# Kernel tuning notes

Measured on AMD Instinct MI355X. Metric: run time of the kernel, lower is better.

Reference implementation:

```python
import jax, jax.numpy as jnp
import numpy as np

N = 50000      # nodes
DEG = 16       # incoming edges per node
E = N * DEG    # edges
F = 256        # nfeat
H = 8          # heads
DH = 32        # nhid // nheads
ALPHA = 0.2    # LeakyReLU negative slope


def setup_inputs() -> dict:
    key = jax.random.key(0)
    ks = jax.random.split(key, 6)
    h = jax.random.normal(ks[0], (N, F), jnp.float32)
    # xavier_uniform-like scale for W (gain 1.414)
    lim_w = 1.414 * np.sqrt(6.0 / (F + DH))
    W = jax.random.uniform(ks[1], (H, F, DH), jnp.float32, -lim_w, lim_w)
    bW = jnp.zeros((H, DH), jnp.float32)
    lim_a = 1.414 * np.sqrt(6.0 / (2 * DH + 1))
    a_src = jax.random.uniform(ks[2], (H, DH), jnp.float32, -lim_a, lim_a)
    a_dst = jax.random.uniform(ks[3], (H, DH), jnp.float32, -lim_a, lim_a)
    a_bias = jnp.zeros((H,), jnp.float32)
    src = jax.random.randint(ks[4], (E,), 0, N, dtype=jnp.int32)
    # every node gets exactly DEG incoming edges (ensures non-empty mailbox)
    dst = jnp.repeat(jnp.arange(N, dtype=jnp.int32), DEG)
    return {"h": h, "W": W, "bW": bW, "a_src": a_src, "a_dst": a_dst,
            "a_bias": a_bias, "src": src, "dst": dst}


def reference(h, W, bW, a_src, a_dst, a_bias, src, dst):
    # per-head projection: Wh[n,h,d]
    Wh = jnp.einsum('nf,hfd->nhd', h, W) + bW
    # decomposed attention linear: a([Wh_src, Wh_dst]) = s1[src] + s2[dst] + b
    s1 = jnp.einsum('nhd,hd->nh', Wh, a_src)   # [N,H]
    s2 = jnp.einsum('nhd,hd->nh', Wh, a_dst)   # [N,H]
    e = jax.nn.leaky_relu(s1[src] + s2[dst] + a_bias, ALPHA)  # [E,H]
    # segment softmax over incoming edges per destination node
    m = jax.ops.segment_max(e, dst, num_segments=N)           # [N,H]
    ex = jnp.exp(e - m[dst])
    denom = jax.ops.segment_sum(ex, dst, num_segments=N)      # [N,H]
    attn = ex / denom[dst]                                    # [E,H]
    # weighted scatter-sum aggregation of source features
    hp = jax.ops.segment_sum(attn[:, :, None] * Wh[src], dst, num_segments=N)  # [N,H,DH]
    # concat heads (matches torch.cat over head outputs)
    return hp.reshape(N, H * DH)
```

## Files before the change

kernel.cpp:

```cpp
#include <hip/hip_runtime.h>

#define NNODES 50000
#define FEAT 256
#define NH 8
#define DHEAD 32
#define DEG 16
#define CDIM 256

typedef __attribute__((ext_vector_type(4))) float floatx4;
typedef __attribute__((ext_vector_type(8))) short shortx8;
typedef __attribute__((ext_vector_type(8))) unsigned short ushortx8;
typedef __attribute__((ext_vector_type(4))) int intx4;
typedef __attribute__((ext_vector_type(4))) _Float16 halfx4;

__device__ __forceinline__ unsigned short f2bf(float f) {
  union { float f; unsigned u; } v; v.f = f;
  unsigned r = v.u + 0x7fffu + ((v.u >> 16) & 1u);
  return (unsigned short)(r >> 16);
}
__device__ __forceinline__ float bf2f(unsigned short b) {
  union { unsigned u; float f; } v; v.u = ((unsigned)b) << 16;
  return v.f;
}

__global__ __launch_bounds__(256) void convert_wt(
    const float* __restrict__ W, unsigned short* __restrict__ Wt2) {
  int t = blockIdx.x * 256 + threadIdx.x;
#pragma unroll
  for (int p = 0; p < 4; ++p) {
    int idx = t * 4 + p;
    int jj = idx & 7;
    int l = (idx >> 3) & 63;
    int kt = (idx >> 9) & 7;
    int cgrp = idx >> 12;
    int c = cgrp * 16 + (l & 15);
    int f = kt * 32 + ((l >> 4) << 3) + jj;
    Wt2[idx] = f2bf(W[(size_t)(c >> 5) * (FEAT * DHEAD) + (size_t)f * DHEAD + (c & 31)]);
  }
}

__global__ __launch_bounds__(256) void gemm_fused(
    const float* __restrict__ h, const unsigned short* __restrict__ Wt2,
    const float* __restrict__ bW, const float* __restrict__ a_src,
    const float* __restrict__ a_dst, const float* __restrict__ a_bias,
    unsigned short* __restrict__ Whb, float* __restrict__ s1g,
    float* __restrict__ s2g) {
  __shared__ unsigned short As2[8 * 2 * 64 * 8];
  const int tid = threadIdx.x;
  const int w = tid >> 6, lane = tid & 63;
  const int mrow = lane & 15, quad = lane >> 4;
  const int row0 = blockIdx.x * 32;

  {
    int r2 = w & 1;
    int ktb = (w >> 1) * 4;
    int grow = row0 + r2 * 16 + mrow;
    if (grow > NNODES - 1) grow = NNODES - 1;
    const float* hp = h + (size_t)grow * FEAT + quad * 8;
#pragma unroll
    for (int ktl = 0; ktl < 4; ++ktl) {
      int kt = ktb + ktl;
      floatx4 v0 = __builtin_nontemporal_load((const floatx4*)(hp + kt * 32));
      floatx4 v1 = __builtin_nontemporal_load((const floatx4*)(hp + kt * 32 + 4));
      shortx8 a8;
      a8[0] = (short)f2bf(v0[0]); a8[1] = (short)f2bf(v0[1]);
      a8[2] = (short)f2bf(v0[2]); a8[3] = (short)f2bf(v0[3]);
      a8[4] = (short)f2bf(v1[0]); a8[5] = (short)f2bf(v1[1]);
      a8[6] = (short)f2bf(v1[2]); a8[7] = (short)f2bf(v1[3]);
      *(shortx8*)&As2[((kt * 2 + r2) * 64 + lane) * 8] = a8;
    }
  }
  __syncthreads();

  floatx4 acc[4][2] = {};
#pragma unroll
  for (int kt = 0; kt < 8; ++kt) {
    shortx8 af[2], bfr[4];
#pragma unroll
    for (int mi = 0; mi < 4; ++mi) {
      int cgrp = w * 4 + mi;
      bfr[mi] = *(const shortx8*)&Wt2[((size_t)(cgrp * 8 + kt) * 64 + lane) * 8];
    }
#pragma unroll
    for (int ni = 0; ni < 2; ++ni)
      af[ni] = *(const shortx8*)&As2[((kt * 2 + ni) * 64 + lane) * 8];
#pragma unroll
    for (int mi = 0; mi < 4; ++mi)
#pragma unroll
      for (int ni = 0; ni < 2; ++ni)
        acc[mi][ni] = __builtin_amdgcn_mfma_f32_16x16x32_bf16(
            bfr[mi], af[ni], acc[mi][ni], 0, 0, 0);
  }

  float4 bw4[4], as4[4], ad4[4];
#pragma unroll
  for (int mi = 0; mi < 4; ++mi) {
    int c0 = w * 64 + mi * 16 + quad * 4;
    bw4[mi] = *(const float4*)&bW[c0];
    as4[mi] = *(const float4*)&a_src[c0];
    ad4[mi] = *(const float4*)&a_dst[c0];
  }
  float ab0 = a_bias[w * 2], ab1 = a_bias[w * 2 + 1];

#pragma unroll
  for (int ni = 0; ni < 2; ++ni) {
    int n = row0 + ni * 16 + mrow;
    bool ok = n < NNODES;
    float p1h0 = 0.f, p1h1 = 0.f, p2h0 = 0.f, p2h1 = 0.f;
#pragma unroll
    for (int mi = 0; mi < 4; ++mi) {
      int c0 = w * 64 + mi * 16 + quad * 4;
      float v0 = acc[mi][ni][0] + bw4[mi].x;
      float v1 = acc[mi][ni][1] + bw4[mi].y;
      float v2 = acc[mi][ni][2] + bw4[mi].z;
      float v3 = acc[mi][ni][3] + bw4[mi].w;
      ushort4 u;
      u.x = f2bf(v0); u.y = f2bf(v1); u.z = f2bf(v2); u.w = f2bf(v3);
      if (ok)
        *(ushort4*)&Whb[(size_t)(c0 >> 5) * ((size_t)NNODES * 32) +
                        (size_t)n * 32 + (c0 & 31)] = u;
      float d1 = v0 * as4[mi].x + v1 * as4[mi].y + v2 * as4[mi].z + v3 * as4[mi].w;
      float d2 = v0 * ad4[mi].x + v1 * ad4[mi].y + v2 * ad4[mi].z + v3 * ad4[mi].w;
      if (mi < 2) { p1h0 += d1; p2h0 += d2; }
      else        { p1h1 += d1; p2h1 += d2; }
    }
    p1h0 += __shfl_xor(p1h0, 16); p1h0 += __shfl_xor(p1h0, 32);
    p1h1 += __shfl_xor(p1h1, 16); p1h1 += __shfl_xor(p1h1, 32);
    p2h0 += __shfl_xor(p2h0, 16); p2h0 += __shfl_xor(p2h0, 32);
    p2h1 += __shfl_xor(p2h1, 16); p2h1 += __shfl_xor(p2h1, 32);
    if (quad == 0 && ok) {
      float2 s1v; s1v.x = p1h0; s1v.y = p1h1;
      float2 s2v; s2v.x = p2h0 + ab0; s2v.y = p2h1 + ab1;
      *(float2*)&s1g[(size_t)n * NH + w * 2] = s1v;
      *(float2*)&s2g[(size_t)n * NH + w * 2] = s2v;
    }
  }
}

__global__ __launch_bounds__(256) void scores(
    const float* __restrict__ s1g, const float* __restrict__ s2g,
    const int* __restrict__ src, _Float16* __restrict__ attw) {
  const int lane = threadIdx.x & 63;
  const int wv = threadIdx.x >> 6;
  const int nl = lane >> 4, e = lane & 15;
  const int n = blockIdx.x * 16 + wv * 4 + nl;

  int s = src[(size_t)n * DEG + e];
  float4 f1a = *(const float4*)&s1g[(size_t)s * NH];
  float4 f1b = *(const float4*)&s1g[(size_t)s * NH + 4];
  float4 f2a = *(const float4*)&s2g[(size_t)n * NH];
  float4 f2b = *(const float4*)&s2g[(size_t)n * NH + 4];

  float sc[8];
  sc[0] = f1a.x + f2a.x; sc[1] = f1a.y + f2a.y;
  sc[2] = f1a.z + f2a.z; sc[3] = f1a.w + f2a.w;
  sc[4] = f1b.x + f2b.x; sc[5] = f1b.y + f2b.y;
  sc[6] = f1b.z + f2b.z; sc[7] = f1b.w + f2b.w;
  float ex[8], sm[8];
#pragma unroll
  for (int hh = 0; hh < 8; ++hh) {
    float t = sc[hh];
    t = t > 0.f ? t : 0.2f * t;
    ex[hh] = __expf(t);
    float su = ex[hh];
    su += __shfl_xor(su, 1);
    su += __shfl_xor(su, 2);
    su += __shfl_xor(su, 4);
    su += __shfl_xor(su, 8);
    sm[hh] = su;
  }
#pragma unroll
  for (int hh = 0; hh < 8; ++hh) {
    float w = ex[hh] * (1.f / sm[hh]);
    attw[(size_t)hh * (NNODES * DEG) + (size_t)n * DEG + e] = (_Float16)w;
  }
}

__global__ __launch_bounds__(256) void aggregate(
    const unsigned short* __restrict__ Whb, const _Float16* __restrict__ attw,
    const int* __restrict__ src, float* __restrict__ out) {
  const int lane = threadIdx.x & 63;
  const int wv = threadIdx.x >> 6;
  const int b = blockIdx.x;
  const int hh = b & 7;
  const int c = lane & 3;
  int n = (b >> 3) * 64 + wv * 16 + (lane >> 2);
  const bool valid = n < NNODES;
  if (!valid) n = NNODES - 1;

  halfx4 w4 = *(const halfx4*)&attw[(size_t)hh * (NNODES * DEG) +
                                    (size_t)n * DEG + c * 4];
  float wA = (float)w4[0], wB = (float)w4[1];
  float wC = (float)w4[2], wD = (float)w4[3];

  const intx4* srow = (const intx4*)&src[(size_t)n * DEG];
  intx4 p0 = srow[0], p1 = srow[1], p2 = srow[2], p3 = srow[3];

  const unsigned short* Wh = Whb + (size_t)hh * ((size_t)NNODES * 32) + c * 8;
  ushortx8 v0  = *(const ushortx8*)&Wh[(size_t)p0.x * 32];
  ushortx8 v1  = *(const ushortx8*)&Wh[(size_t)p0.y * 32];
  ushortx8 v2  = *(const ushortx8*)&Wh[(size_t)p0.z * 32];
  ushortx8 v3  = *(const ushortx8*)&Wh[(size_t)p0.w * 32];
  ushortx8 v4  = *(const ushortx8*)&Wh[(size_t)p1.x * 32];
  ushortx8 v5  = *(const ushortx8*)&Wh[(size_t)p1.y * 32];
  ushortx8 v6  = *(const ushortx8*)&Wh[(size_t)p1.z * 32];
  ushortx8 v7  = *(const ushortx8*)&Wh[(size_t)p1.w * 32];
  ushortx8 v8  = *(const ushortx8*)&Wh[(size_t)p2.x * 32];
  ushortx8 v9  = *(const ushortx8*)&Wh[(size_t)p2.y * 32];
  ushortx8 v10 = *(const ushortx8*)&Wh[(size_t)p2.z * 32];
  ushortx8 v11 = *(const ushortx8*)&Wh[(size_t)p2.w * 32];
  ushortx8 v12 = *(const ushortx8*)&Wh[(size_t)p3.x * 32];
  ushortx8 v13 = *(const ushortx8*)&Wh[(size_t)p3.y * 32];
  ushortx8 v14 = *(const ushortx8*)&Wh[(size_t)p3.z * 32];
  ushortx8 v15 = *(const ushortx8*)&Wh[(size_t)p3.w * 32];

  float acc0 = 0.f, acc1 = 0.f, acc2 = 0.f, acc3 = 0.f;
  float acc4 = 0.f, acc5 = 0.f, acc6 = 0.f, acc7 = 0.f;
#define ACC8(WK, VV)                                               \
  {                                                                \
    float wk = (WK);                                               \
    acc0 += wk * bf2f(VV[0]); acc1 += wk * bf2f(VV[1]);            \
    acc2 += wk * bf2f(VV[2]); acc3 += wk * bf2f(VV[3]);            \
    acc4 += wk * bf2f(VV[4]); acc5 += wk * bf2f(VV[5]);            \
    acc6 += wk * bf2f(VV[6]); acc7 += wk * bf2f(VV[7]);            \
  }
#define STEP4(CC, VA, VB, VC, VD)                                  \
  {                                                                \
    int sl = (lane & 60) | CC;                                     \
    ACC8(__shfl(wA, sl), VA); ACC8(__shfl(wB, sl), VB);            \
    ACC8(__shfl(wC, sl), VC); ACC8(__shfl(wD, sl), VD);            \
  }
  STEP4(0, v0, v1, v2, v3)
  STEP4(1, v4, v5, v6, v7)
  STEP4(2, v8, v9, v10, v11)
  STEP4(3, v12, v13, v14, v15)
#undef STEP4
#undef ACC8

  if (valid) {
    float* op = &out[(size_t)n * CDIM + hh * 32 + c * 8];
    floatx4 o0, o1;
    o0.x = acc0; o0.y = acc1; o0.z = acc2; o0.w = acc3;
    o1.x = acc4; o1.y = acc5; o1.z = acc6; o1.w = acc7;
    __builtin_nontemporal_store(o0, (floatx4*)op);
    __builtin_nontemporal_store(o1, (floatx4*)(op + 4));
  }
}

extern "C" void kernel_launch(void* const* d_in, const int* in_sizes, int n_in,
                              void* d_out, int out_size, void* d_ws, size_t ws_size,
                              hipStream_t stream) {
  const float* h = (const float*)d_in[0];
  const float* W = (const float*)d_in[1];
  const float* bW = (const float*)d_in[2];
  const float* a_src = (const float*)d_in[3];
  const float* a_dst = (const float*)d_in[4];
  const float* a_bias = (const float*)d_in[5];
  const int* src = (const int*)d_in[6];
  float* out = (float*)d_out;

  unsigned short* Whb = (unsigned short*)d_ws;
  unsigned short* Wt2 = Whb + (size_t)NNODES * CDIM;
  float* s1g = (float*)(Wt2 + CDIM * FEAT);
  float* s2g = s1g + (size_t)NNODES * NH;
  _Float16* attw = (_Float16*)(s2g + (size_t)NNODES * NH);

  convert_wt<<<64, 256, 0, stream>>>(W, Wt2);
  gemm_fused<<<(NNODES + 31) / 32, 256, 0, stream>>>(h, Wt2, bW, a_src, a_dst,
                                                     a_bias, Whb, s1g, s2g);
  scores<<<NNODES / 16, 256, 0, stream>>>(s1g, s2g, src, attw);
  aggregate<<<782 * 8, 256, 0, stream>>>(Whb, attw, src, out);
}
```

Before: 178.7 us.

## Retile projection GEMM to 64 rows per block with 8 waves, one head each

The fused projection GEMM now processes 64 node rows per block with 512 threads (8 waves). Each wave owns one head's 32 output columns across four 16-row tiles, where before each wave owned 64 columns across two row tiles. Each W fragment loaded from global memory is therefore reused across more rows, halving the number of W fetches per node. The epilogue becomes a single-head reduction per wave. The trade-offs are fewer, larger blocks, more LDS per block, and scalar instead of float2 stores for s1/s2.

```diff
diff --git a/kernel.cpp b/kernel.cpp
--- a/kernel.cpp
+++ b/kernel.cpp
@@ -39,22 +39,22 @@
   }
 }
 
-__global__ __launch_bounds__(256) void gemm_fused(
+__global__ __launch_bounds__(512) void gemm_fused(
     const float* __restrict__ h, const unsigned short* __restrict__ Wt2,
     const float* __restrict__ bW, const float* __restrict__ a_src,
     const float* __restrict__ a_dst, const float* __restrict__ a_bias,
     unsigned short* __restrict__ Whb, float* __restrict__ s1g,
     float* __restrict__ s2g) {
-  __shared__ unsigned short As2[8 * 2 * 64 * 8];
+  __shared__ unsigned short As2[8 * 4 * 64 * 8];
   const int tid = threadIdx.x;
   const int w = tid >> 6, lane = tid & 63;
   const int mrow = lane & 15, quad = lane >> 4;
-  const int row0 = blockIdx.x * 32;
+  const int row0 = blockIdx.x * 64;
 
   {
-    int r2 = w & 1;
-    int ktb = (w >> 1) * 4;
-    int grow = row0 + r2 * 16 + mrow;
+    int r4 = w & 3;
+    int ktb = (w >> 2) * 4;
+    int grow = row0 + r4 * 16 + mrow;
     if (grow > NNODES - 1) grow = NNODES - 1;
     const float* hp = h + (size_t)grow * FEAT + quad * 8;
 #pragma unroll
@@ -67,72 +67,65 @@
       a8[2] = (short)f2bf(v0[2]); a8[3] = (short)f2bf(v0[3]);
       a8[4] = (short)f2bf(v1[0]); a8[5] = (short)f2bf(v1[1]);
       a8[6] = (short)f2bf(v1[2]); a8[7] = (short)f2bf(v1[3]);
-      *(shortx8*)&As2[((kt * 2 + r2) * 64 + lane) * 8] = a8;
+      *(shortx8*)&As2[((kt * 4 + r4) * 64 + lane) * 8] = a8;
     }
   }
   __syncthreads();
 
-  floatx4 acc[4][2] = {};
+  floatx4 acc[2][4] = {};
 #pragma unroll
   for (int kt = 0; kt < 8; ++kt) {
-    shortx8 af[2], bfr[4];
-#pragma unroll
-    for (int mi = 0; mi < 4; ++mi) {
-      int cgrp = w * 4 + mi;
+    shortx8 af[4], bfr[2];
+#pragma unroll
+    for (int mi = 0; mi < 2; ++mi) {
+      int cgrp = w * 2 + mi;
       bfr[mi] = *(const shortx8*)&Wt2[((size_t)(cgrp * 8 + kt) * 64 + lane) * 8];
     }
 #pragma unroll
-    for (int ni = 0; ni < 2; ++ni)
-      af[ni] = *(const shortx8*)&As2[((kt * 2 + ni) * 64 + lane) * 8];
-#pragma unroll
-    for (int mi = 0; mi < 4; ++mi)
-#pragma unroll
-      for (int ni = 0; ni < 2; ++ni)
+    for (int ni = 0; ni < 4; ++ni)
+      af[ni] = *(const shortx8*)&As2[((kt * 4 + ni) * 64 + lane) * 8];
+#pragma unroll
+    for (int mi = 0; mi < 2; ++mi)
+#pragma unroll
+      for (int ni = 0; ni < 4; ++ni)
         acc[mi][ni] = __builtin_amdgcn_mfma_f32_16x16x32_bf16(
             bfr[mi], af[ni], acc[mi][ni], 0, 0, 0);
   }
 
-  float4 bw4[4], as4[4], ad4[4];
-#pragma unroll
-  for (int mi = 0; mi < 4; ++mi) {
-    int c0 = w * 64 + mi * 16 + quad * 4;
+  float4 bw4[2], as4[2], ad4[2];
+#pragma unroll
+  for (int mi = 0; mi < 2; ++mi) {
+    int c0 = w * 32 + mi * 16 + quad * 4;
     bw4[mi] = *(const float4*)&bW[c0];
     as4[mi] = *(const float4*)&a_src[c0];
     ad4[mi] = *(const float4*)&a_dst[c0];
   }
-  float ab0 = a_bias[w * 2], ab1 = a_bias[w * 2 + 1];
-
-#pragma unroll
-  for (int ni = 0; ni < 2; ++ni) {
+  float ab = a_bias[w];
+  unsigned short* Whs = Whb + (size_t)w * ((size_t)NNODES * 32);
+
+#pragma unroll
+  for (int ni = 0; ni < 4; ++ni) {
     int n = row0 + ni * 16 + mrow;
     bool ok = n < NNODES;
-    float p1h0 = 0.f, p1h1 = 0.f, p2h0 = 0.f, p2h1 = 0.f;
-#pragma unroll
-    for (int mi = 0; mi < 4; ++mi) {
-      int c0 = w * 64 + mi * 16 + quad * 4;
+    float p1 = 0.f, p2 = 0.f;
+#pragma unroll
+    for (int mi = 0; mi < 2; ++mi) {
+      int cl = mi * 16 + quad * 4;
       float v0 = acc[mi][ni][0] + bw4[mi].x;
       float v1 = acc[mi][ni][1] + bw4[mi].y;
       float v2 = acc[mi][ni][2] + bw4[mi].z;
       float v3 = acc[mi][ni][3] + bw4[mi].w;
       ushort4 u;
       u.x = f2bf(v0); u.y = f2bf(v1); u.z = f2bf(v2); u.w = f2bf(v3);
-      if (ok)
-        *(ushort4*)&Whb[(size_t)(c0 >> 5) * ((size_t)NNODES * 32) +
-                        (size_t)n * 32 + (c0 & 31)] = u;
-      float d1 = v0 * as4[mi].x + v1 * as4[mi].y + v2 * as4[mi].z + v3 * as4[mi].w;
-      float d2 = v0 * ad4[mi].x + v1 * ad4[mi].y + v2 * ad4[mi].z + v3 * ad4[mi].w;
-      if (mi < 2) { p1h0 += d1; p2h0 += d2; }
-      else        { p1h1 += d1; p2h1 += d2; }
-    }
-    p1h0 += __shfl_xor(p1h0, 16); p1h0 += __shfl_xor(p1h0, 32);
-    p1h1 += __shfl_xor(p1h1, 16); p1h1 += __shfl_xor(p1h1, 32);
-    p2h0 += __shfl_xor(p2h0, 16); p2h0 += __shfl_xor(p2h0, 32);
-    p2h1 += __shfl_xor(p2h1, 16); p2h1 += __shfl_xor(p2h1, 32);
+      if (ok) *(ushort4*)&Whs[(size_t)n * 32 + cl] = u;
+      p1 += v0 * as4[mi].x + v1 * as4[mi].y + v2 * as4[mi].z + v3 * as4[mi].w;
+      p2 += v0 * ad4[mi].x + v1 * ad4[mi].y + v2 * ad4[mi].z + v3 * ad4[mi].w;
+    }
+    p1 += __shfl_xor(p1, 16); p1 += __shfl_xor(p1, 32);
+    p2 += __shfl_xor(p2, 16); p2 += __shfl_xor(p2, 32);
     if (quad == 0 && ok) {
-      float2 s1v; s1v.x = p1h0; s1v.y = p1h1;
-      float2 s2v; s2v.x = p2h0 + ab0; s2v.y = p2h1 + ab1;
-      *(float2*)&s1g[(size_t)n * NH + w * 2] = s1v;
-      *(float2*)&s2g[(size_t)n * NH + w * 2] = s2v;
+      s1g[(size_t)n * NH + w] = p1;
+      s2g[(size_t)n * NH + w] = p2 + ab;
     }
   }
 }
@@ -266,7 +259,7 @@
   _Float16* attw = (_Float16*)(s2g + (size_t)NNODES * NH);
 
   convert_wt<<<64, 256, 0, stream>>>(W, Wt2);
-  gemm_fused<<<(NNODES + 31) / 32, 256, 0, stream>>>(h, Wt2, bW, a_src, a_dst,
+  gemm_fused<<<(NNODES + 63) / 64, 512, 0, stream>>>(h, Wt2, bW, a_src, a_dst,
                                                      a_bias, Whb, s1g, s2g);
   scores<<<NNODES / 16, 256, 0, stream>>>(s1g, s2g, src, attw);
   aggregate<<<782 * 8, 256, 0, stream>>>(Whb, attw, src, out);
```

After: 175.5 us. About the same (-1.8%).
